# Kernel tuning notes

Measured on AMD Instinct MI355X. Metric: run time of the kernel, lower is better.

The kernel has to match this reference:

```python
import jax, jax.numpy as jnp
import numpy as np

B, N = 1, 1024
NODE, PAIR, H = 384, 128, 12
DQS, DQP, DVS, DVP = 16, 4, 16, 8
SCALAR_SCALE = (3 * DQS) ** -0.5
POINT_SCALE = (3 * DQP * (9 * 2 ** 0.5)) ** -0.5
PAIR_SCALE = 3 ** -0.5
LN_EPS = 1e-5
NORM_EPS = 1e-8


def layer_norm(x, g, b):
    m = jnp.mean(x, axis=-1, keepdims=True)
    v = jnp.var(x, axis=-1, keepdims=True)
    return (x - m) * jax.lax.rsqrt(v + LN_EPS) * g + b


def heads_first(x, h):  # b n (h d) -> b h n d
    b, n, hd = x.shape
    return x.reshape(b, n, h, hd // h).transpose(0, 2, 1, 3)


def heads_last(x):  # b h n d -> b n (h d)
    b, h, n, d = x.shape
    return x.transpose(0, 2, 1, 3).reshape(b, n, h * d)


def setup_inputs() -> dict:
    key = jax.random.key(0)
    ks = jax.random.split(key, 8)
    node_feats = jax.random.normal(ks[0], (B, N, NODE), jnp.float32)
    rot_raw = jax.random.normal(ks[1], (B, N, 3, 3), jnp.float32)
    rot, _ = jnp.linalg.qr(rot_raw)  # valid rotations (orthonormal)
    trans = jax.random.normal(ks[2], (B, N, 3), jnp.float32) * 10.0
    pair_feats = jax.random.normal(ks[3], (B, N, N, PAIR), jnp.float32)
    mask = jnp.ones((B, N), dtype=bool)
    W_pb = jax.random.normal(ks[4], (H, PAIR), jnp.float32) * 0.02
    W_qkv = jax.random.normal(ks[5], (2 * H * DQS + H * DVS + 2 * H * DQP * 3 + H * DVP * 3, NODE), jnp.float32) * 0.02
    W_out = jax.random.normal(ks[6], (NODE, H * (PAIR + DVS + 4 * DVP)), jnp.float32) * 0.02
    b_out = jnp.zeros((NODE,), jnp.float32)
    point_weights = jnp.log(jnp.exp(jnp.ones((1, H, 1, 1), jnp.float32)) - 1.0)
    return dict(node_feats=node_feats, rot=rot, trans=trans, pair_feats=pair_feats, mask=mask,
                ln_s_g=jnp.ones((NODE,), jnp.float32), ln_s_b=jnp.zeros((NODE,), jnp.float32),
                ln_p_g=jnp.ones((PAIR,), jnp.float32), ln_p_b=jnp.zeros((PAIR,), jnp.float32),
                W_pb=W_pb, W_qkv=W_qkv, point_weights=point_weights, W_out=W_out, b_out=b_out)


def reference(node_feats, rot, trans, pair_feats, mask, ln_s_g, ln_s_b, ln_p_g, ln_p_b,
              W_pb, W_qkv, point_weights, W_out, b_out):
    b, n = node_feats.shape[:2]
    nf = layer_norm(node_feats, ln_s_g, ln_s_b)
    pf = layer_norm(pair_feats, ln_p_g, ln_p_b)
    pair_bias = jnp.einsum('bijp,hp->bhij', pf, W_pb)

    qkv = jnp.einsum('bnd,od->bno', nf, W_qkv)
    sizes = [H * DQS, H * DQS, H * DVS, H * DQP * 3, H * DQP * 3, H * DVP * 3]
    offs = np.cumsum([0] + sizes)
    q_s, k_s, v_s, q_p, k_p, v_p = [qkv[..., offs[i]:offs[i + 1]] for i in range(6)]

    q_s, k_s, v_s = (heads_first(x, H) for x in (q_s, k_s, v_s))  # b h n d
    scalar_logits = jnp.einsum('bhid,bhjd->bhij', q_s, k_s)

    def to_global_points(x, d):
        x = x.reshape(b, n, H * d, 3)                                # ... (d c) -> ... d c
        x = jnp.einsum('birc,bimc->bimr', rot, x) + trans[:, :, None, :]  # rigids.apply
        return x.reshape(b, n, H, d, 3).transpose(0, 2, 1, 3, 4)     # b h n d 3

    qp = to_global_points(q_p, DQP)
    kp = to_global_points(k_p, DQP)
    vp = to_global_points(v_p, DVP)

    # dist_attn: -sum((q_i - k_j)^2) over (d, c), expanded to avoid bhijdc tensor
    q2 = jnp.sum(qp * qp, axis=(-1, -2))  # b h i
    k2 = jnp.sum(kp * kp, axis=(-1, -2))  # b h j
    qk = jnp.einsum('bhidc,bhjdc->bhij', qp, kp)
    point_logits = -(q2[:, :, :, None] + k2[:, :, None, :] - 2.0 * qk)
    point_logits = point_logits * jax.nn.softplus(point_weights)

    mask2d = mask[:, None, :, None] & mask[:, None, None, :]  # b 1 i j
    min_val = jnp.finfo(point_logits.dtype).min
    point_logits = jnp.where(mask2d, point_logits, min_val)
    scalar_logits = jnp.where(mask2d, scalar_logits, min_val)
    pair_bias = jnp.where(mask2d, pair_bias, min_val)

    logits = (SCALAR_SCALE * scalar_logits + POINT_SCALE * point_logits + PAIR_SCALE * pair_bias)
    attn = jax.nn.softmax(logits, axis=-1)

    res_scalar = jnp.einsum('bhij,bhjd->bhid', attn, v_s)
    res_pair = jnp.einsum('bhij,bijd->bhid', attn, pf)
    res_pt = jnp.einsum('bhij,bhjdc->bhidc', attn, vp)

    # rigids.apply_inverse: R^T (x - t)
    rp = res_pt.transpose(0, 2, 1, 3, 4).reshape(b, n, H * DVP, 3)
    rp = jnp.einsum('bicr,bimc->bimr', rot, rp - trans[:, :, None, :])
    res_pt = rp.reshape(b, n, H, DVP, 3).transpose(0, 2, 1, 3, 4)  # b h n d 3

    res_pt_norm = jnp.sqrt(jnp.sum(res_pt * res_pt, axis=-1) + NORM_EPS)  # b h n d
    res_pt_flat = res_pt.reshape(b, H, n, DVP * 3)

    out = jnp.concatenate([heads_last(res_scalar), heads_last(res_pt_flat),
                           heads_last(res_pt_norm), heads_last(res_pair)], axis=-1)
    return jnp.einsum('bno,do->bnd', out, W_out) + b_out
```

## Files before the change

### kernel.cpp

```cpp
#include <hip/hip_runtime.h>

#define N_TOK 1024
#define NODE  384
#define PAIR  128
#define H     12
#define QKV_DIM 1152
#define OUT_CAT 2112
#define JT    32

#define OFF_NF   0
#define OFF_QKV  (OFF_NF  + N_TOK*NODE)
#define OFF_GQP  (OFF_QKV + N_TOK*QKV_DIM)
#define OFF_GKP  (OFF_GQP + N_TOK*144)
#define OFF_GVP  (OFF_GKP + N_TOK*144)
#define OFF_Q2   (OFF_GVP + N_TOK*288)
#define OFF_K2   (OFF_Q2  + N_TOK*H)
#define OFF_X    (OFF_K2  + N_TOK*H)

__global__ void ln_node_kernel(const float* __restrict__ x, const float* __restrict__ g,
                               const float* __restrict__ b, float* __restrict__ y) {
    int n = blockIdx.x, t = threadIdx.x;
    const float* row = x + (size_t)n * NODE;
    float v[6];
    float s = 0.f, q = 0.f;
#pragma unroll
    for (int w = 0; w < 6; ++w) { v[w] = row[t + 64*w]; s += v[w]; q += v[w]*v[w]; }
#pragma unroll
    for (int m = 1; m < 64; m <<= 1) { s += __shfl_xor(s, m, 64); q += __shfl_xor(q, m, 64); }
    float mean = s * (1.f/NODE);
    float var  = q * (1.f/NODE) - mean*mean;
    float rs   = rsqrtf(var + 1e-5f);
#pragma unroll
    for (int w = 0; w < 6; ++w) {
        int k = t + 64*w;
        y[(size_t)n*NODE + k] = (v[w]-mean)*rs*g[k] + b[k];
    }
}

template<int BM, int BN, int TM, int TN, int KC>
__global__ void gemm_nt(const float* __restrict__ A, const float* __restrict__ B,
                        const float* __restrict__ bias, float* __restrict__ C,
                        int M, int N, int K) {
    constexpr int TX = BN / TN, TY = BM / TM;
    constexpr int THREADS = TX * TY;
    static_assert(BM * KC / 4 == THREADS && BN * KC / 4 == THREADS, "load mapping");
    __shared__ float As[KC][BM + 4];
    __shared__ float Bs[KC][BN + 4];
    const int t  = threadIdx.x;
    const int m0 = blockIdx.x * BM, n0 = blockIdx.y * BN;
    const int tn = t % TX, tm = t / TX;
    constexpr int LPR = KC / 4;
    const int lr = t / LPR, lk = t % LPR;
    float acc[TM][TN] = {};
    for (int k0 = 0; k0 < K; k0 += KC) {
        float4 a4 = *(const float4*)(A + (size_t)(m0 + lr) * K + k0 + lk*4);
        float4 b4 = *(const float4*)(B + (size_t)(n0 + lr) * K + k0 + lk*4);
        __syncthreads();
        As[lk*4+0][lr] = a4.x; As[lk*4+1][lr] = a4.y; As[lk*4+2][lr] = a4.z; As[lk*4+3][lr] = a4.w;
        Bs[lk*4+0][lr] = b4.x; Bs[lk*4+1][lr] = b4.y; Bs[lk*4+2][lr] = b4.z; Bs[lk*4+3][lr] = b4.w;
        __syncthreads();
#pragma unroll
        for (int k = 0; k < KC; ++k) {
            float a[TM], b[TN];
            if constexpr (TM == 4) { *(float4*)a = *(const float4*)&As[k][tm*TM]; }
            else                   { *(float2*)a = *(const float2*)&As[k][tm*TM]; }
            if constexpr (TN == 4) { *(float4*)b = *(const float4*)&Bs[k][tn*TN]; }
            else                   { *(float2*)b = *(const float2*)&Bs[k][tn*TN]; }
#pragma unroll
            for (int r = 0; r < TM; ++r)
#pragma unroll
                for (int c = 0; c < TN; ++c) acc[r][c] += a[r] * b[c];
        }
    }
#pragma unroll
    for (int r = 0; r < TM; ++r)
#pragma unroll
        for (int c = 0; c < TN; ++c) {
            int m = m0 + tm*TM + r, n = n0 + tn*TN + c;
            float o = acc[r][c] + (bias ? bias[n] : 0.f);
            C[(size_t)m * N + n] = o;
        }
}

__global__ void prep_points(const float* __restrict__ qkv, const float* __restrict__ rot,
                            const float* __restrict__ trans,
                            float* __restrict__ gqp, float* __restrict__ gkp,
                            float* __restrict__ gvp, float* __restrict__ q2a,
                            float* __restrict__ k2a) {
    int n = blockIdx.x, t = threadIdx.x;
    __shared__ float sq[144], sk[144];
    float R[9], T[3];
#pragma unroll
    for (int k = 0; k < 9; ++k) R[k] = rot[(size_t)n*9 + k];
#pragma unroll
    for (int c = 0; c < 3; ++c) T[c] = trans[(size_t)n*3 + c];
    const float* row = qkv + (size_t)n * QKV_DIM;
    if (t < 48) {
        int m = t;
        float x0 = row[576 + m*3], x1 = row[576 + m*3 + 1], x2 = row[576 + m*3 + 2];
#pragma unroll
        for (int r = 0; r < 3; ++r) {
            float g = R[r*3+0]*x0 + R[r*3+1]*x1 + R[r*3+2]*x2 + T[r];
            gqp[(size_t)n*144 + m*3 + r] = g; sq[m*3 + r] = g;
        }
    } else if (t < 96) {
        int m = t - 48;
        float x0 = row[720 + m*3], x1 = row[720 + m*3 + 1], x2 = row[720 + m*3 + 2];
#pragma unroll
        for (int r = 0; r < 3; ++r) {
            float g = R[r*3+0]*x0 + R[r*3+1]*x1 + R[r*3+2]*x2 + T[r];
            gkp[(size_t)n*144 + m*3 + r] = g; sk[m*3 + r] = g;
        }
    } else if (t < 192) {
        int m = t - 96;
        float x0 = row[864 + m*3], x1 = row[864 + m*3 + 1], x2 = row[864 + m*3 + 2];
#pragma unroll
        for (int r = 0; r < 3; ++r)
            gvp[(size_t)n*288 + m*3 + r] = R[r*3+0]*x0 + R[r*3+1]*x1 + R[r*3+2]*x2 + T[r];
    }
    __syncthreads();
    if (t < 12) {
        float s = 0.f;
#pragma unroll
        for (int u = 0; u < 12; ++u) { float g = sq[t*12 + u]; s += g*g; }
        q2a[(size_t)n*H + t] = s;
    } else if (t < 24) {
        int h = t - 12; float s = 0.f;
#pragma unroll
        for (int u = 0; u < 12; ++u) { float g = sk[h*12 + u]; s += g*g; }
        k2a[(size_t)n*H + h] = s;
    }
}

__global__ __launch_bounds__(384)
void ipa_attn(const float* __restrict__ pair, const float* __restrict__ lpg,
              const float* __restrict__ lpb, const float* __restrict__ wpb,
              const float* __restrict__ pw,  const float* __restrict__ qkv,
              const float* __restrict__ gqp, const float* __restrict__ q2a,
              const float* __restrict__ gkp, const float* __restrict__ k2a,
              const float* __restrict__ gvp, const float* __restrict__ rot,
              const float* __restrict__ trans, float* __restrict__ X) {
    __shared__ float s_pf[2][JT][132];
    __shared__ float s_wpb[H][PAIR];
    __shared__ float s_g[PAIR], s_b[PAIR];

    const int t = threadIdx.x;
    const int h = t >> 5, q = t & 31;
    const int i0 = blockIdx.x * 2;

    ((float4*)s_wpb)[t] = ((const float4*)wpb)[t];
    if (t < 32) {
        ((float4*)s_g)[t] = ((const float4*)lpg)[t];
        ((float4*)s_b)[t] = ((const float4*)lpb)[t];
    }

    float qs[2][16], qp[2][12], q2v[2];
#pragma unroll
    for (int i = 0; i < 2; ++i) {
        const float* qr = qkv + (size_t)(i0+i)*QKV_DIM + h*16;
#pragma unroll
        for (int d = 0; d < 16; ++d) qs[i][d] = qr[d];
        const float* pr = gqp + (size_t)(i0+i)*144 + h*12;
#pragma unroll
        for (int m = 0; m < 12; ++m) qp[i][m] = pr[m];
        q2v[i] = q2a[(size_t)(i0+i)*H + h];
    }
    const float spw = log1pf(__expf(pw[h]));
    const float SS  = 0.14433756729740643f;
    const float PSC = -0.08091538742f * spw;
    const float PB  = 0.5773502691896258f;

    float m_[2] = { -3.0e38f, -3.0e38f };
    float l_[2] = { 0.f, 0.f };
    float accP[2][4] = {};
    float accS[2] = { 0.f, 0.f };
    float accT[2] = { 0.f, 0.f };

    for (int j0 = 0; j0 < N_TOK; j0 += JT) {
        __syncthreads();
#pragma unroll
        for (int pass = 0; pass < 2; ++pass) {
            int row = pass*48 + (t >> 3);
            if (row < 64) {
                int i = row >> 5, jj = row & 31, lane = t & 7;
                const float* src = pair + ((size_t)(i0+i)*N_TOK + j0 + jj)*PAIR + lane*16;
                float f[16];
                *(float4*)&f[0]  = ((const float4*)src)[0];
                *(float4*)&f[4]  = ((const float4*)src)[1];
                *(float4*)&f[8]  = ((const float4*)src)[2];
                *(float4*)&f[12] = ((const float4*)src)[3];
                float s = 0.f, qq = 0.f;
#pragma unroll
                for (int k = 0; k < 16; ++k) { s += f[k]; qq += f[k]*f[k]; }
#pragma unroll
                for (int mm = 1; mm < 8; mm <<= 1) {
                    s  += __shfl_xor(s,  mm, 8);
                    qq += __shfl_xor(qq, mm, 8);
                }
                float mean = s * (1.f/128.f);
                float var  = qq * (1.f/128.f) - mean*mean;
                float rs   = rsqrtf(var + 1e-5f);
                float* dst = &s_pf[i][jj][lane*16];
#pragma unroll
                for (int k = 0; k < 16; ++k)
                    f[k] = (f[k]-mean)*rs*s_g[lane*16+k] + s_b[lane*16+k];
                ((float4*)dst)[0] = *(float4*)&f[0];
                ((float4*)dst)[1] = *(float4*)&f[4];
                ((float4*)dst)[2] = *(float4*)&f[8];
                ((float4*)dst)[3] = *(float4*)&f[12];
            }
        }
        __syncthreads();

        float lg0, lg1;
        {
            const float4* wrow = (const float4*)&s_wpb[h][0];
            const float4* p0r  = (const float4*)&s_pf[0][q][0];
            const float4* p1r  = (const float4*)&s_pf[1][q][0];
            float bias0 = 0.f, bias1 = 0.f;
#pragma unroll 8
            for (int k = 0; k < 32; ++k) {
                float4 w = wrow[k], a = p0r[k], b = p1r[k];
                bias0 += w.x*a.x + w.y*a.y + w.z*a.z + w.w*a.w;
                bias1 += w.x*b.x + w.y*b.y + w.z*b.z + w.w*b.w;
            }
            int j = j0 + q;
            const float* kr = qkv + (size_t)j*QKV_DIM + 192 + h*16;
            float sl0 = 0.f, sl1 = 0.f;
#pragma unroll
            for (int d = 0; d < 16; ++d) { float kv = kr[d]; sl0 += qs[0][d]*kv; sl1 += qs[1][d]*kv; }
            const float* kpr = gkp + (size_t)j*144 + h*12;
            float qk0 = 0.f, qk1 = 0.f;
#pragma unroll
            for (int m = 0; m < 12; ++m) { float kv = kpr[m]; qk0 += qp[0][m]*kv; qk1 += qp[1][m]*kv; }
            float k2v = k2a[(size_t)j*H + h];
            float d0 = q2v[0] + k2v - 2.f*qk0;
            float d1 = q2v[1] + k2v - 2.f*qk1;
            lg0 = SS*sl0 + PSC*d0 + PB*bias0;
            lg1 = SS*sl1 + PSC*d1 + PB*bias1;
        }

        float p0, p1;
        {
            float mx = lg0;
#pragma unroll
            for (int mm = 1; mm < 32; mm <<= 1) mx = fmaxf(mx, __shfl_xor(mx, mm, 32));
            float mnew = fmaxf(m_[0], mx);
            float al = __expf(m_[0] - mnew);
            p0 = __expf(lg0 - mnew);
            float s = p0;
#pragma unroll
            for (int mm = 1; mm < 32; mm <<= 1) s += __shfl_xor(s, mm, 32);
            l_[0] = l_[0]*al + s; m_[0] = mnew;
            accP[0][0]*=al; accP[0][1]*=al; accP[0][2]*=al; accP[0][3]*=al;
            accS[0]*=al; accT[0]*=al;
        }
        {
            float mx = lg1;
#pragma unroll
            for (int mm = 1; mm < 32; mm <<= 1) mx = fmaxf(mx, __shfl_xor(mx, mm, 32));
            float mnew = fmaxf(m_[1], mx);
            float al = __expf(m_[1] - mnew);
            p1 = __expf(lg1 - mnew);
            float s = p1;
#pragma unroll
            for (int mm = 1; mm < 32; mm <<= 1) s += __shfl_xor(s, mm, 32);
            l_[1] = l_[1]*al + s; m_[1] = mnew;
            accP[1][0]*=al; accP[1][1]*=al; accP[1][2]*=al; accP[1][3]*=al;
            accS[1]*=al; accT[1]*=al;
        }

        const float* vsbase = qkv + (size_t)j0*QKV_DIM + 384 + h*16 + q;
        const float* gvbase = gvp + (size_t)j0*288 + h*24 + q;
#pragma unroll 4
        for (int jj = 0; jj < JT; ++jj) {
            float pj0 = __shfl(p0, jj, 32);
            float pj1 = __shfl(p1, jj, 32);
            float4 a = *(const float4*)&s_pf[0][jj][q*4];
            float4 b = *(const float4*)&s_pf[1][jj][q*4];
            accP[0][0] += pj0*a.x; accP[0][1] += pj0*a.y; accP[0][2] += pj0*a.z; accP[0][3] += pj0*a.w;
            accP[1][0] += pj1*b.x; accP[1][1] += pj1*b.y; accP[1][2] += pj1*b.z; accP[1][3] += pj1*b.w;
            if (q < 16) { float v = vsbase[(size_t)jj*QKV_DIM]; accS[0] += pj0*v; accS[1] += pj1*v; }
            if (q < 24) { float g = gvbase[jj*288];             accT[0] += pj0*g; accT[1] += pj1*g; }
        }
    }

#pragma unroll
    for (int i = 0; i < 2; ++i) {
        int n = i0 + i;
        float inv = 1.f / l_[i];
        float* Xr = X + (size_t)n * OUT_CAT;
        if (q < 16) Xr[h*16 + q] = accS[i]*inv;
        float4 pr;
        pr.x = accP[i][0]*inv; pr.y = accP[i][1]*inv; pr.z = accP[i][2]*inv; pr.w = accP[i][3]*inv;
        *(float4*)&Xr[576 + h*128 + q*4] = pr;

        float v = accT[i]*inv;
        int dp3 = (q/3)*3;
        float v0 = __shfl(v, dp3 + 0, 32);
        float v1 = __shfl(v, dp3 + 1, 32);
        float v2 = __shfl(v, dp3 + 2, 32);
        int r = q - dp3;
        float rp = rot[(size_t)n*9 + 0*3 + r]*(v0 - trans[(size_t)n*3 + 0])
                 + rot[(size_t)n*9 + 1*3 + r]*(v1 - trans[(size_t)n*3 + 1])
                 + rot[(size_t)n*9 + 2*3 + r]*(v2 - trans[(size_t)n*3 + 2]);
        if (q < 24) Xr[192 + h*24 + q] = rp;
        int s0 = (q < 8) ? q*3 : 0;
        float r0 = __shfl(rp, s0 + 0, 32);
        float r1 = __shfl(rp, s0 + 1, 32);
        float r2 = __shfl(rp, s0 + 2, 32);
        if (q < 8) Xr[480 + h*8 + q] = sqrtf(r0*r0 + r1*r1 + r2*r2 + 1e-8f);
    }
}

extern "C" void kernel_launch(void* const* d_in, const int* in_sizes, int n_in,
                              void* d_out, int out_size, void* d_ws, size_t ws_size,
                              hipStream_t stream) {
    const float* node  = (const float*)d_in[0];
    const float* rot   = (const float*)d_in[1];
    const float* trans = (const float*)d_in[2];
    const float* pair  = (const float*)d_in[3];
    const float* lsg  = (const float*)d_in[5];
    const float* lsb  = (const float*)d_in[6];
    const float* lpg  = (const float*)d_in[7];
    const float* lpb  = (const float*)d_in[8];
    const float* wpb  = (const float*)d_in[9];
    const float* wqkv = (const float*)d_in[10];
    const float* pw   = (const float*)d_in[11];
    const float* wout = (const float*)d_in[12];
    const float* bout = (const float*)d_in[13];

    float* ws  = (float*)d_ws;
    float* NF  = ws + OFF_NF;
    float* QKV = ws + OFF_QKV;
    float* GQP = ws + OFF_GQP;
    float* GKP = ws + OFF_GKP;
    float* GVP = ws + OFF_GVP;
    float* Q2  = ws + OFF_Q2;
    float* K2A = ws + OFF_K2;
    float* Xc  = ws + OFF_X;

    ln_node_kernel<<<N_TOK, 64, 0, stream>>>(node, lsg, lsb, NF);
    gemm_nt<64,64,4,4,16><<<dim3(N_TOK/64, QKV_DIM/64), 256, 0, stream>>>(
        NF, wqkv, nullptr, QKV, N_TOK, QKV_DIM, NODE);
    prep_points<<<N_TOK, 256, 0, stream>>>(QKV, rot, trans, GQP, GKP, GVP, Q2, K2A);
    ipa_attn<<<N_TOK/2, 384, 0, stream>>>(pair, lpg, lpb, wpb, pw, QKV,
                                          GQP, Q2, GKP, K2A, GVP, rot, trans, Xc);
    gemm_nt<32,32,2,2,32><<<dim3(N_TOK/32, NODE/32), 256, 0, stream>>>(
        Xc, wout, bout, (float*)d_out, N_TOK, NODE, OUT_CAT);
}
```

Baseline: 2.027 ms.

## Rewrite IPA attention with bf16 MFMA for pair bias and pair aggregation

Replaces the attention kernel with a 512-thread version that converts the normalized pair tile to bf16 in swizzled shared memory. It uses 16x16x32 bf16 MFMA both for the pair-bias projection and for the attention-weighted pair aggregation. The j-tile grows to 64, and the work is split across waves per (head, query) pair, with softmax rescale factors passed through shared memory. This aims to cut the FP32 ALU cost of the two 128-wide pair contractions. In exchange it lowers precision to bf16 and adds more barriers per tile.

```diff
diff --git a/kernel.cpp b/kernel.cpp
--- a/kernel.cpp
+++ b/kernel.cpp
@@ -6,7 +6,6 @@
 #define H     12
 #define QKV_DIM 1152
 #define OUT_CAT 2112
-#define JT    32
 
 #define OFF_NF   0
 #define OFF_QKV  (OFF_NF  + N_TOK*NODE)
@@ -16,6 +15,15 @@
 #define OFF_Q2   (OFF_GVP + N_TOK*288)
 #define OFF_K2   (OFF_Q2  + N_TOK*H)
 #define OFF_X    (OFF_K2  + N_TOK*H)
+
+typedef __attribute__((ext_vector_type(8))) short s8v;
+typedef __attribute__((ext_vector_type(4))) float f4a;
+
+static __device__ __forceinline__ unsigned short f2b(float x) {
+    unsigned u = __builtin_bit_cast(unsigned, x);
+    unsigned r = (u + 0x7FFF + ((u >> 16) & 1)) >> 16;
+    return (unsigned short)r;
+}
 
 __global__ void ln_node_kernel(const float* __restrict__ x, const float* __restrict__ g,
                                const float* __restrict__ b, float* __restrict__ y) {
@@ -132,184 +140,274 @@
     }
 }
 
-__global__ __launch_bounds__(384)
-void ipa_attn(const float* __restrict__ pair, const float* __restrict__ lpg,
-              const float* __restrict__ lpb, const float* __restrict__ wpb,
-              const float* __restrict__ pw,  const float* __restrict__ qkv,
-              const float* __restrict__ gqp, const float* __restrict__ q2a,
-              const float* __restrict__ gkp, const float* __restrict__ k2a,
-              const float* __restrict__ gvp, const float* __restrict__ rot,
-              const float* __restrict__ trans, float* __restrict__ X) {
-    __shared__ float s_pf[2][JT][132];
-    __shared__ float s_wpb[H][PAIR];
-    __shared__ float s_g[PAIR], s_b[PAIR];
-
-    const int t = threadIdx.x;
-    const int h = t >> 5, q = t & 31;
-    const int i0 = blockIdx.x * 2;
-
-    ((float4*)s_wpb)[t] = ((const float4*)wpb)[t];
-    if (t < 32) {
-        ((float4*)s_g)[t] = ((const float4*)lpg)[t];
-        ((float4*)s_b)[t] = ((const float4*)lpb)[t];
-    }
-
-    float qs[2][16], qp[2][12], q2v[2];
-#pragma unroll
-    for (int i = 0; i < 2; ++i) {
-        const float* qr = qkv + (size_t)(i0+i)*QKV_DIM + h*16;
-#pragma unroll
-        for (int d = 0; d < 16; ++d) qs[i][d] = qr[d];
-        const float* pr = gqp + (size_t)(i0+i)*144 + h*12;
-#pragma unroll
-        for (int m = 0; m < 12; ++m) qp[i][m] = pr[m];
-        q2v[i] = q2a[(size_t)(i0+i)*H + h];
-    }
-    const float spw = log1pf(__expf(pw[h]));
-    const float SS  = 0.14433756729740643f;
-    const float PSC = -0.08091538742f * spw;
-    const float PB  = 0.5773502691896258f;
-
-    float m_[2] = { -3.0e38f, -3.0e38f };
-    float l_[2] = { 0.f, 0.f };
-    float accP[2][4] = {};
-    float accS[2] = { 0.f, 0.f };
-    float accT[2] = { 0.f, 0.f };
-
-    for (int j0 = 0; j0 < N_TOK; j0 += JT) {
-        __syncthreads();
-#pragma unroll
-        for (int pass = 0; pass < 2; ++pass) {
-            int row = pass*48 + (t >> 3);
-            if (row < 64) {
-                int i = row >> 5, jj = row & 31, lane = t & 7;
-                const float* src = pair + ((size_t)(i0+i)*N_TOK + j0 + jj)*PAIR + lane*16;
-                float f[16];
-                *(float4*)&f[0]  = ((const float4*)src)[0];
-                *(float4*)&f[4]  = ((const float4*)src)[1];
-                *(float4*)&f[8]  = ((const float4*)src)[2];
-                *(float4*)&f[12] = ((const float4*)src)[3];
-                float s = 0.f, qq = 0.f;
-#pragma unroll
-                for (int k = 0; k < 16; ++k) { s += f[k]; qq += f[k]*f[k]; }
-#pragma unroll
-                for (int mm = 1; mm < 8; mm <<= 1) {
-                    s  += __shfl_xor(s,  mm, 8);
-                    qq += __shfl_xor(qq, mm, 8);
+__global__ __launch_bounds__(512, 4)
+void ipa_attn2(const float* __restrict__ pair, const float* __restrict__ lpg,
+               const float* __restrict__ lpb, const float* __restrict__ wpb,
+               const float* __restrict__ pw,  const float* __restrict__ qkv,
+               const float* __restrict__ gqp, const float* __restrict__ q2a,
+               const float* __restrict__ gkp, const float* __restrict__ k2a,
+               const float* __restrict__ gvp, const float* __restrict__ rot,
+               const float* __restrict__ trans, float* __restrict__ X) {
+    __shared__ __align__(16) unsigned short s_pf[128][136];
+    __shared__ __align__(16) unsigned short s_at[2][16][72];
+    __shared__ __align__(16) float s_af[2][12][68];
+    __shared__ __align__(16) float s_lgb[128][21];
+    __shared__ float s_alpha[2][16];
+    __shared__ float s_linv[2][16];
+    __shared__ __align__(16) float s_q[2][12][32];
+    __shared__ __align__(16) unsigned short s_wf[4][64][8];
+
+    const int t    = threadIdx.x;
+    const int lane = t & 63, w = t >> 6;
+    const int quad = (t >> 4) & 3, nn = t & 15;
+    const int i0   = blockIdx.x * 2;
+
+    const float SS = 0.14433756729740643f;
+    const float PB = 0.5773502691896258f;
+
+    for (int idx = t; idx < 696; idx += 512) {
+        int pp = idx / 29, e = idx % 29;
+        int i = pp / 12, h = pp % 12;
+        float v;
+        if (e < 16)      v = qkv[(size_t)(i0+i)*QKV_DIM + h*16 + e];
+        else if (e < 28) v = gqp[(size_t)(i0+i)*144 + h*12 + (e-16)];
+        else             v = q2a[(size_t)(i0+i)*H + h];
+        s_q[i][h][e] = v;
+    }
+    if (t < 64) {
+        int qd = t >> 4, hq = t & 15;
+#pragma unroll
+        for (int k = 0; k < 4; ++k) {
+            s8v v;
+#pragma unroll
+            for (int e = 0; e < 8; ++e) {
+                int d = k*32 + qd*8 + e;
+                float x = (hq < 12) ? wpb[hq*128 + d] : 0.f;
+                v[e] = (short)f2b(x);
+            }
+            *(s8v*)&s_wf[k][t][0] = v;
+        }
+    }
+
+    int pc_h[3], pc_i[3];
+    float pscv[3];
+#pragma unroll
+    for (int c = 0; c < 3; ++c) {
+        int p = w*3 + c;
+        pc_h[c] = p >> 1; pc_i[c] = p & 1;
+        float sp = log1pf(__expf(pw[pc_h[c]]));
+        pscv[c] = -0.08091538742f * sp;
+    }
+    float mC[3] = {-3.0e38f, -3.0e38f, -3.0e38f};
+    float lC[3] = {0.f, 0.f, 0.f};
+
+    const int hh = (t < 480) ? t / 40 : 0;
+    const int dd = (t < 480) ? t % 40 : 0;
+    const float* vbase = (dd < 16) ? (qkv + 384 + hh*16 + dd)
+                                   : (gvp + hh*24 + (dd-16));
+    const int vstr = (dd < 16) ? QKV_DIM : 288;
+    float sA0 = 0.f, sA1 = 0.f;
+
+    const int i_r = w & 1, nt0 = w >> 1;
+    f4a accR[2] = {{0.f,0.f,0.f,0.f},{0.f,0.f,0.f,0.f}};
+
+    const int rowA = t >> 2, l4 = t & 3;
+    const int ipA = rowA >> 6, jjA = rowA & 63;
+    const int mswA = (rowA >> 3) & 7;
+
+    for (int j0 = 0; j0 < N_TOK; j0 += 64) {
+        {
+            const float* src = pair + ((size_t)(i0 + ipA)*N_TOK + (j0 + jjA))*PAIR + l4*32;
+            float f[32];
+#pragma unroll
+            for (int u = 0; u < 8; ++u) *(float4*)&f[u*4] = *(const float4*)&src[u*4];
+            float s = 0.f, qq = 0.f;
+#pragma unroll
+            for (int u = 0; u < 32; ++u) { s += f[u]; qq += f[u]*f[u]; }
+            s  += __shfl_xor(s, 1, 4);  s  += __shfl_xor(s, 2, 4);
+            qq += __shfl_xor(qq, 1, 4); qq += __shfl_xor(qq, 2, 4);
+            float mean = s * (1.f/128.f);
+            float var  = qq * (1.f/128.f) - mean*mean;
+            float rs   = rsqrtf(var + 1e-5f);
+#pragma unroll
+            for (int w2 = 0; w2 < 4; ++w2) {
+                int c = l4*4 + w2;
+                float4 g0 = *(const float4*)&lpg[c*8], g1 = *(const float4*)&lpg[c*8+4];
+                float4 b0 = *(const float4*)&lpb[c*8], b1 = *(const float4*)&lpb[c*8+4];
+                float gg[8] = {g0.x,g0.y,g0.z,g0.w,g1.x,g1.y,g1.z,g1.w};
+                float bb[8] = {b0.x,b0.y,b0.z,b0.w,b1.x,b1.y,b1.z,b1.w};
+                s8v v;
+#pragma unroll
+                for (int e = 0; e < 8; ++e) {
+                    float y = (f[w2*8 + e] - mean)*rs*gg[e] + bb[e];
+                    v[e] = (short)f2b(y);
                 }
-                float mean = s * (1.f/128.f);
-                float var  = qq * (1.f/128.f) - mean*mean;
-                float rs   = rsqrtf(var + 1e-5f);
-                float* dst = &s_pf[i][jj][lane*16];
-#pragma unroll
-                for (int k = 0; k < 16; ++k)
-                    f[k] = (f[k]-mean)*rs*s_g[lane*16+k] + s_b[lane*16+k];
-                ((float4*)dst)[0] = *(float4*)&f[0];
-                ((float4*)dst)[1] = *(float4*)&f[4];
-                ((float4*)dst)[2] = *(float4*)&f[8];
-                ((float4*)dst)[3] = *(float4*)&f[12];
-            }
-        }
-        __syncthreads();
-
-        float lg0, lg1;
+                *(s8v*)&s_pf[rowA][((c ^ mswA) << 3)] = v;
+            }
+        }
+        __syncthreads();
+
+        if (w < 4) {
+#pragma unroll
+            for (int mi = 0; mi < 2; ++mi) {
+                int mt = w + mi*4;
+                int row = mt*16 + nn;
+                int msw = (row >> 3) & 7;
+                f4a acc = {0.f,0.f,0.f,0.f};
+#pragma unroll
+                for (int k = 0; k < 4; ++k) {
+                    s8v a  = *(const s8v*)&s_pf[row][(((k*4 + quad) ^ msw) << 3)];
+                    s8v wf = *(const s8v*)&s_wf[k][lane][0];
+                    acc = __builtin_amdgcn_mfma_f32_16x16x32_bf16(a, wf, acc, 0, 0, 0);
+                }
+#pragma unroll
+                for (int r = 0; r < 4; ++r)
+                    s_lgb[mt*16 + quad*4 + r][nn] = acc[r];
+            }
+        }
+
+        float lg[3];
         {
-            const float4* wrow = (const float4*)&s_wpb[h][0];
-            const float4* p0r  = (const float4*)&s_pf[0][q][0];
-            const float4* p1r  = (const float4*)&s_pf[1][q][0];
-            float bias0 = 0.f, bias1 = 0.f;
-#pragma unroll 8
-            for (int k = 0; k < 32; ++k) {
-                float4 w = wrow[k], a = p0r[k], b = p1r[k];
-                bias0 += w.x*a.x + w.y*a.y + w.z*a.z + w.w*a.w;
-                bias1 += w.x*b.x + w.y*b.y + w.z*b.z + w.w*b.w;
-            }
-            int j = j0 + q;
-            const float* kr = qkv + (size_t)j*QKV_DIM + 192 + h*16;
-            float sl0 = 0.f, sl1 = 0.f;
-#pragma unroll
-            for (int d = 0; d < 16; ++d) { float kv = kr[d]; sl0 += qs[0][d]*kv; sl1 += qs[1][d]*kv; }
-            const float* kpr = gkp + (size_t)j*144 + h*12;
-            float qk0 = 0.f, qk1 = 0.f;
-#pragma unroll
-            for (int m = 0; m < 12; ++m) { float kv = kpr[m]; qk0 += qp[0][m]*kv; qk1 += qp[1][m]*kv; }
-            float k2v = k2a[(size_t)j*H + h];
-            float d0 = q2v[0] + k2v - 2.f*qk0;
-            float d1 = q2v[1] + k2v - 2.f*qk1;
-            lg0 = SS*sl0 + PSC*d0 + PB*bias0;
-            lg1 = SS*sl1 + PSC*d1 + PB*bias1;
-        }
-
-        float p0, p1;
+            int hprev = -1;
+            float ks[16], kpv[12], k2v = 0.f;
+            const int jg = j0 + lane;
+#pragma unroll
+            for (int c = 0; c < 3; ++c) {
+                const int hc = pc_h[c], ic = pc_i[c];
+                if (hc != hprev) {
+                    const float* kr = qkv + (size_t)jg*QKV_DIM + 192 + hc*16;
+                    *(float4*)&ks[0]  = *(const float4*)&kr[0];
+                    *(float4*)&ks[4]  = *(const float4*)&kr[4];
+                    *(float4*)&ks[8]  = *(const float4*)&kr[8];
+                    *(float4*)&ks[12] = *(const float4*)&kr[12];
+                    const float* pr = gkp + (size_t)jg*144 + hc*12;
+                    *(float4*)&kpv[0] = *(const float4*)&pr[0];
+                    *(float4*)&kpv[4] = *(const float4*)&pr[4];
+                    *(float4*)&kpv[8] = *(const float4*)&pr[8];
+                    k2v = k2a[(size_t)jg*H + hc];
+                    hprev = hc;
+                }
+                const float* qv = &s_q[ic][hc][0];
+                float sl = 0.f;
+#pragma unroll
+                for (int d = 0; d < 16; ++d) sl += qv[d]*ks[d];
+                float qk = 0.f;
+#pragma unroll
+                for (int m = 0; m < 12; ++m) qk += qv[16+m]*kpv[m];
+                float d2 = qv[28] + k2v - 2.f*qk;
+                lg[c] = SS*sl + pscv[c]*d2;
+            }
+        }
+        __syncthreads();
+
+#pragma unroll
+        for (int c = 0; c < 3; ++c) {
+            const int hc = pc_h[c], ic = pc_i[c];
+            float L = lg[c] + PB * s_lgb[ic*64 + lane][hc];
+            float mx = L;
+#pragma unroll
+            for (int m = 1; m < 64; m <<= 1) mx = fmaxf(mx, __shfl_xor(mx, m, 64));
+            float mnew = fmaxf(mC[c], mx);
+            float al = __expf(mC[c] - mnew);
+            float p  = __expf(L - mnew);
+            float sm = p;
+#pragma unroll
+            for (int m = 1; m < 64; m <<= 1) sm += __shfl_xor(sm, m, 64);
+            lC[c] = lC[c]*al + sm;
+            mC[c] = mnew;
+            s_at[ic][hc][lane] = f2b(p);
+            s_af[ic][hc][lane] = p;
+            if (lane == 0) s_alpha[ic][hc] = al;
+        }
+        __syncthreads();
+
         {
-            float mx = lg0;
-#pragma unroll
-            for (int mm = 1; mm < 32; mm <<= 1) mx = fmaxf(mx, __shfl_xor(mx, mm, 32));
-            float mnew = fmaxf(m_[0], mx);
-            float al = __expf(m_[0] - mnew);
-            p0 = __expf(lg0 - mnew);
-            float s = p0;
-#pragma unroll
-            for (int mm = 1; mm < 32; mm <<= 1) s += __shfl_xor(s, mm, 32);
-            l_[0] = l_[0]*al + s; m_[0] = mnew;
-            accP[0][0]*=al; accP[0][1]*=al; accP[0][2]*=al; accP[0][3]*=al;
-            accS[0]*=al; accT[0]*=al;
-        }
-        {
-            float mx = lg1;
-#pragma unroll
-            for (int mm = 1; mm < 32; mm <<= 1) mx = fmaxf(mx, __shfl_xor(mx, mm, 32));
-            float mnew = fmaxf(m_[1], mx);
-            float al = __expf(m_[1] - mnew);
-            p1 = __expf(lg1 - mnew);
-            float s = p1;
-#pragma unroll
-            for (int mm = 1; mm < 32; mm <<= 1) s += __shfl_xor(s, mm, 32);
-            l_[1] = l_[1]*al + s; m_[1] = mnew;
-            accP[1][0]*=al; accP[1][1]*=al; accP[1][2]*=al; accP[1][3]*=al;
-            accS[1]*=al; accT[1]*=al;
-        }
-
-        const float* vsbase = qkv + (size_t)j0*QKV_DIM + 384 + h*16 + q;
-        const float* gvbase = gvp + (size_t)j0*288 + h*24 + q;
+            float4 al4 = *(const float4*)&s_alpha[i_r][quad*4];
+            accR[0][0]*=al4.x; accR[0][1]*=al4.y; accR[0][2]*=al4.z; accR[0][3]*=al4.w;
+            accR[1][0]*=al4.x; accR[1][1]*=al4.y; accR[1][2]*=al4.z; accR[1][3]*=al4.w;
+            s8v af0 = *(const s8v*)&s_at[i_r][nn][quad*8];
+            s8v af1 = *(const s8v*)&s_at[i_r][nn][32 + quad*8];
+#pragma unroll
+            for (int idx = 0; idx < 2; ++idx) {
+                int d = (nt0 + idx*4)*16 + nn;
+                int ch = d >> 3, dl = d & 7;
+#pragma unroll
+                for (int s_ = 0; s_ < 2; ++s_) {
+                    int msw = (s_*4 + quad) & 7;
+                    const unsigned short* bp =
+                        &s_pf[i_r*64 + s_*32 + quad*8][((ch ^ msw) << 3) | dl];
+                    s8v bf;
+#pragma unroll
+                    for (int e = 0; e < 8; ++e) bf[e] = (short)bp[e*136];
+                    accR[idx] = __builtin_amdgcn_mfma_f32_16x16x32_bf16(
+                        (s_ == 0 ? af0 : af1), bf, accR[idx], 0, 0, 0);
+                }
+            }
+        }
+        if (t < 480) {
+            float a0 = s_alpha[0][hh], a1 = s_alpha[1][hh];
+            sA0 *= a0; sA1 *= a1;
+            const float* vr = vbase + (size_t)j0 * vstr;
 #pragma unroll 4
-        for (int jj = 0; jj < JT; ++jj) {
-            float pj0 = __shfl(p0, jj, 32);
-            float pj1 = __shfl(p1, jj, 32);
-            float4 a = *(const float4*)&s_pf[0][jj][q*4];
-            float4 b = *(const float4*)&s_pf[1][jj][q*4];
-            accP[0][0] += pj0*a.x; accP[0][1] += pj0*a.y; accP[0][2] += pj0*a.z; accP[0][3] += pj0*a.w;
-            accP[1][0] += pj1*b.x; accP[1][1] += pj1*b.y; accP[1][2] += pj1*b.z; accP[1][3] += pj1*b.w;
-            if (q < 16) { float v = vsbase[(size_t)jj*QKV_DIM]; accS[0] += pj0*v; accS[1] += pj1*v; }
-            if (q < 24) { float g = gvbase[jj*288];             accT[0] += pj0*g; accT[1] += pj1*g; }
-        }
-    }
-
-#pragma unroll
-    for (int i = 0; i < 2; ++i) {
+            for (int jb = 0; jb < 16; ++jb) {
+                float4 p0 = *(const float4*)&s_af[0][hh][jb*4];
+                float4 p1 = *(const float4*)&s_af[1][hh][jb*4];
+                float v0 = vr[(jb*4+0)*vstr];
+                float v1 = vr[(jb*4+1)*vstr];
+                float v2 = vr[(jb*4+2)*vstr];
+                float v3 = vr[(jb*4+3)*vstr];
+                sA0 += p0.x*v0 + p0.y*v1 + p0.z*v2 + p0.w*v3;
+                sA1 += p1.x*v0 + p1.y*v1 + p1.z*v2 + p1.w*v3;
+            }
+        }
+        __syncthreads();
+    }
+
+#pragma unroll
+    for (int c = 0; c < 3; ++c)
+        if (lane == 0) s_linv[pc_i[c]][pc_h[c]] = 1.f / lC[c];
+    __syncthreads();
+
+    float* s_ptf = &s_lgb[0][0];
+    if (t < 480) {
+        float li0 = s_linv[0][hh], li1 = s_linv[1][hh];
+        if (dd < 16) {
+            X[(size_t)i0*OUT_CAT + hh*16 + dd]     = sA0*li0;
+            X[(size_t)(i0+1)*OUT_CAT + hh*16 + dd] = sA1*li1;
+        } else {
+            s_ptf[(0*12 + hh)*24 + (dd-16)] = sA0*li0;
+            s_ptf[(12  + hh)*24 + (dd-16)] = sA1*li1;
+        }
+    }
+    {
+        float4 li4 = *(const float4*)&s_linv[i_r][quad*4];
+        float liarr[4] = {li4.x, li4.y, li4.z, li4.w};
+#pragma unroll
+        for (int idx = 0; idx < 2; ++idx) {
+            int dcol = (nt0 + idx*4)*16 + nn;
+#pragma unroll
+            for (int r = 0; r < 4; ++r) {
+                int h = quad*4 + r;
+                if (h < 12)
+                    X[(size_t)(i0+i_r)*OUT_CAT + 576 + h*128 + dcol] = accR[idx][r]*liarr[r];
+            }
+        }
+    }
+    __syncthreads();
+    if (t < 192) {
+        int i = t / 96, rem = t % 96, h = rem >> 3, dp = rem & 7;
         int n = i0 + i;
-        float inv = 1.f / l_[i];
-        float* Xr = X + (size_t)n * OUT_CAT;
-        if (q < 16) Xr[h*16 + q] = accS[i]*inv;
-        float4 pr;
-        pr.x = accP[i][0]*inv; pr.y = accP[i][1]*inv; pr.z = accP[i][2]*inv; pr.w = accP[i][3]*inv;
-        *(float4*)&Xr[576 + h*128 + q*4] = pr;
-
-        float v = accT[i]*inv;
-        int dp3 = (q/3)*3;
-        float v0 = __shfl(v, dp3 + 0, 32);
-        float v1 = __shfl(v, dp3 + 1, 32);
-        float v2 = __shfl(v, dp3 + 2, 32);
-        int r = q - dp3;
-        float rp = rot[(size_t)n*9 + 0*3 + r]*(v0 - trans[(size_t)n*3 + 0])
-                 + rot[(size_t)n*9 + 1*3 + r]*(v1 - trans[(size_t)n*3 + 1])
-                 + rot[(size_t)n*9 + 2*3 + r]*(v2 - trans[(size_t)n*3 + 2]);
-        if (q < 24) Xr[192 + h*24 + q] = rp;
-        int s0 = (q < 8) ? q*3 : 0;
-        float r0 = __shfl(rp, s0 + 0, 32);
-        float r1 = __shfl(rp, s0 + 1, 32);
-        float r2 = __shfl(rp, s0 + 2, 32);
-        if (q < 8) Xr[480 + h*8 + q] = sqrtf(r0*r0 + r1*r1 + r2*r2 + 1e-8f);
+        float v0 = s_ptf[(i*12+h)*24 + dp*3 + 0] - trans[n*3+0];
+        float v1 = s_ptf[(i*12+h)*24 + dp*3 + 1] - trans[n*3+1];
+        float v2 = s_ptf[(i*12+h)*24 + dp*3 + 2] - trans[n*3+2];
+        float r0 = rot[n*9+0]*v0 + rot[n*9+3]*v1 + rot[n*9+6]*v2;
+        float r1 = rot[n*9+1]*v0 + rot[n*9+4]*v1 + rot[n*9+7]*v2;
+        float r2 = rot[n*9+2]*v0 + rot[n*9+5]*v1 + rot[n*9+8]*v2;
+        float* Xr = X + (size_t)n*OUT_CAT;
+        Xr[192 + h*24 + dp*3 + 0] = r0;
+        Xr[192 + h*24 + dp*3 + 1] = r1;
+        Xr[192 + h*24 + dp*3 + 2] = r2;
+        Xr[480 + h*8 + dp] = sqrtf(r0*r0 + r1*r1 + r2*r2 + 1e-8f);
     }
 }
 
@@ -344,8 +442,8 @@
     gemm_nt<64,64,4,4,16><<<dim3(N_TOK/64, QKV_DIM/64), 256, 0, stream>>>(
         NF, wqkv, nullptr, QKV, N_TOK, QKV_DIM, NODE);
     prep_points<<<N_TOK, 256, 0, stream>>>(QKV, rot, trans, GQP, GKP, GVP, Q2, K2A);
-    ipa_attn<<<N_TOK/2, 384, 0, stream>>>(pair, lpg, lpb, wpb, pw, QKV,
-                                          GQP, Q2, GKP, K2A, GVP, rot, trans, Xc);
+    ipa_attn2<<<N_TOK/2, 512, 0, stream>>>(pair, lpg, lpb, wpb, pw, QKV,
+                                           GQP, Q2, GKP, K2A, GVP, rot, trans, Xc);
     gemm_nt<32,32,2,2,32><<<dim3(N_TOK/32, NODE/32), 256, 0, stream>>>(
         Xc, wout, bout, (float*)d_out, N_TOK, NODE, OUT_CAT);
 }
```

Measured after the change: 1.725 ms. -14.9%, faster.
